# Optimization experiments

Measured on AMD Instinct MI355X. Metric: run time of the kernel, lower is better.

## Reference

```python
import jax, jax.numpy as jnp
import numpy as np

COMMITMENT = 1e-4
EPS = 1e-12  # F.normalize eps


def setup_inputs() -> dict:
    key = jax.random.key(0)
    k1, k2 = jax.random.split(key)
    b, h, l, d, c = 4, 8, 4096, 64, 512
    x = jax.random.normal(k1, (b, h, l, d), dtype=jnp.float32)
    means = jax.random.normal(k2, (h, c, d), dtype=jnp.float32)
    return {"x": x, "means": means}


def reference(x, means):
    # x: [b,h,l,d], means: [h,c,d]
    h = means.shape[0]
    # F.normalize(x, 2, dim=-1): x / max(||x||, eps)
    norm = jnp.linalg.norm(x, axis=-1, keepdims=True)
    xn = x / jnp.maximum(norm, EPS)
    # cosine similarity to cluster centers: [b,h,l,c]
    dists = jnp.einsum('bhld,hcd->bhlc', xn, means)
    buckets = jnp.argmax(dists, axis=-1)  # [b,h,l]
    # batched_index_select of means per (head, bucket): [b,h,l,d]
    routed_means = means[jnp.arange(h)[None, :, None], buckets]
    loss = jnp.mean((xn - routed_means) ** 2) * COMMITMENT
    return dists, loss
```

## Files before the change

### kernel.cpp

```cpp
#include <hip/hip_runtime.h>
#include <hip/hip_bf16.h>

#define NB 4
#define NH 8
#define NL 4096
#define ND 64
#define NC 512
#define TILE_L 64
#define EPSV 1e-12f
#define COMMITV 0.0001f
#define NBLOCKS (NB * NH * (NL / TILE_L))

typedef __attribute__((ext_vector_type(8))) short bf16x8;
typedef __attribute__((ext_vector_type(4))) float f32x4;

__device__ __forceinline__ unsigned bfpack(float a, float b) {
    unsigned ua = __float_as_uint(a);
    unsigned ub = __float_as_uint(b);
    ua = (ua + 0x7fffu + ((ua >> 16) & 1u)) >> 16;
    ub = (ub + 0x7fffu + ((ub >> 16) & 1u)) & 0xffff0000u;
    return (ua & 0xffffu) | ub;
}

__global__ __launch_bounds__(256, 2) void kmeans_kernel(
    const float* __restrict__ x, const float* __restrict__ means,
    float* __restrict__ dists, float* __restrict__ part)
{
    __shared__ alignas(16) unsigned short m_lds[NC * ND];
    __shared__ alignas(16) unsigned short x_lds[TILE_L * ND];
    __shared__ float msq[NC];
    __shared__ float sn2[TILE_L];
    __shared__ float wsum[4];

    const int t = threadIdx.x;
    const int ltiles = NL / TILE_L;
    const int bh = blockIdx.x / ltiles;
    const int l0 = (blockIdx.x % ltiles) * TILE_L;
    const int h  = bh & (NH - 1);

    const float4* mp = (const float4*)(means + (size_t)h * NC * ND);
    #pragma unroll 4
    for (int i = 0; i < 32; ++i) {
        int f4 = t + i * 256;
        float4 v = mp[f4];
        int row = f4 >> 4;
        int q = f4 & 15;
        float ss = v.x * v.x + v.y * v.y + v.z * v.z + v.w * v.w;
        ss += __shfl_xor(ss, 1); ss += __shfl_xor(ss, 2);
        ss += __shfl_xor(ss, 4); ss += __shfl_xor(ss, 8);
        if ((t & 15) == 0) msq[row] = ss;
        unsigned lo = bfpack(v.x, v.y), hi = bfpack(v.z, v.w);
        int byte = row * 128 + ((q * 8) ^ ((row & 7) << 4));
        *(unsigned long long*)((char*)m_lds + byte) =
            (unsigned long long)lo | ((unsigned long long)hi << 32);
    }

    const float4* xp = (const float4*)(x + ((size_t)bh * NL + l0) * ND);
    #pragma unroll
    for (int i = 0; i < 4; ++i) {
        int f4 = t + i * 256;
        float4 v = xp[f4];
        int row = f4 >> 4;
        int q = f4 & 15;
        float ss = v.x * v.x + v.y * v.y + v.z * v.z + v.w * v.w;
        ss += __shfl_xor(ss, 1); ss += __shfl_xor(ss, 2);
        ss += __shfl_xor(ss, 4); ss += __shfl_xor(ss, 8);
        float inv = 1.0f / fmaxf(sqrtf(ss), EPSV);
        if ((t & 15) == 0) sn2[row] = ss * inv * inv;
        float ax = v.x * inv, ay = v.y * inv, az = v.z * inv, aw = v.w * inv;
        int byte = row * 128 + ((q * 8) ^ ((row & 7) << 4));
        *(unsigned long long*)((char*)x_lds + byte) =
            (unsigned long long)bfpack(ax, ay) | ((unsigned long long)bfpack(az, aw) << 32);
    }
    __syncthreads();

    const int wave = t >> 6, lane = t & 63;
    const int r16 = lane & 15, g = lane >> 4;

    const int arow = wave * 16 + r16;
    const char* xb = (const char*)x_lds + arow * 128;
    const int sw = (arow & 7) << 4;
    bf16x8 a0 = *(const bf16x8*)(xb + ((g * 16) ^ sw));
    bf16x8 a1 = *(const bf16x8*)(xb + ((64 + g * 16) ^ sw));

    float mx[4]; int mi[4];
    #pragma unroll
    for (int r = 0; r < 4; ++r) { mx[r] = -1e30f; mi[r] = 0; }

    const size_t obase = ((size_t)bh * NL + l0 + wave * 16) * NC;

    #pragma unroll 4
    for (int c0 = 0; c0 < NC; c0 += 16) {
        int brow = c0 + r16;
        const char* mb = (const char*)m_lds + brow * 128;
        const int bsw = (brow & 7) << 4;
        bf16x8 b0 = *(const bf16x8*)(mb + ((g * 16) ^ bsw));
        bf16x8 b1 = *(const bf16x8*)(mb + ((64 + g * 16) ^ bsw));
        f32x4 acc = {0.f, 0.f, 0.f, 0.f};
        acc = __builtin_amdgcn_mfma_f32_16x16x32_bf16(a0, b0, acc, 0, 0, 0);
        acc = __builtin_amdgcn_mfma_f32_16x16x32_bf16(a1, b1, acc, 0, 0, 0);
        #pragma unroll
        for (int r = 0; r < 4; ++r) {
            float v = acc[r];
            dists[obase + (size_t)(g * 4 + r) * NC + (c0 + r16)] = v;
            if (v > mx[r]) { mx[r] = v; mi[r] = c0 + r16; }
        }
    }

    #pragma unroll
    for (int s = 1; s < 16; s <<= 1) {
        #pragma unroll
        for (int r = 0; r < 4; ++r) {
            float ov = __shfl_xor(mx[r], s);
            int   oi = __shfl_xor(mi[r], s);
            if (ov > mx[r] || (ov == mx[r] && oi < mi[r])) { mx[r] = ov; mi[r] = oi; }
        }
    }

    float sacc = 0.f;
    #pragma unroll
    for (int r = 0; r < 4; ++r)
        sacc += sn2[wave * 16 + g * 4 + r] - 2.f * mx[r] + msq[mi[r]];
    if (r16 != 0) sacc = 0.f;
    sacc += __shfl_xor(sacc, 16);
    sacc += __shfl_xor(sacc, 32);
    if (lane == 0) wsum[wave] = sacc;
    __syncthreads();
    if (t == 0) part[blockIdx.x] = wsum[0] + wsum[1] + wsum[2] + wsum[3];
}

__global__ __launch_bounds__(256) void loss_reduce(
    const float* __restrict__ part, float* __restrict__ loss)
{
    __shared__ float w[4];
    const int t = threadIdx.x;
    float s = 0.f;
    #pragma unroll
    for (int i = 0; i < NBLOCKS / 256; ++i) s += part[t + i * 256];
    s += __shfl_xor(s, 1);  s += __shfl_xor(s, 2);  s += __shfl_xor(s, 4);
    s += __shfl_xor(s, 8);  s += __shfl_xor(s, 16); s += __shfl_xor(s, 32);
    if ((t & 63) == 0) w[t >> 6] = s;
    __syncthreads();
    if (t == 0)
        loss[0] = (w[0] + w[1] + w[2] + w[3]) *
                  (COMMITV / (float)((size_t)NB * NH * NL * ND));
}

extern "C" void kernel_launch(void* const* d_in, const int* in_sizes, int n_in,
                              void* d_out, int out_size, void* d_ws, size_t ws_size,
                              hipStream_t stream) {
    const float* x = (const float*)d_in[0];
    const float* means = (const float*)d_in[1];
    float* dists = (float*)d_out;
    float* loss = dists + (size_t)NB * NH * NL * NC;
    float* part = (float*)d_ws;

    dim3 grid(NBLOCKS);
    dim3 block(256);
    kmeans_kernel<<<grid, block, 0, stream>>>(x, means, dists, part);
    loss_reduce<<<dim3(1), block, 0, stream>>>(part, loss);
}
```

Baseline: 362.3 us.

## Double L-tile per block, load x fragments directly to registers, nontemporal dists stores

Each block now covers 128 rows with 512 threads, which halves how often the per-head means tile is reloaded and converted into LDS. The x rows are read straight from global memory into MFMA A-fragments, normalised in registers with a cross-lane reduction, so the x LDS staging buffer is gone. The dists output is written with nontemporal stores to cut cache pollution from the large write stream. LDS use per block stays near 66KB, so occupancy may be limited, and the direct x loads are less coalesced.

Result: faster. 330.2 us (-8.9%).

```diff
diff --git a/kernel.cpp b/kernel.cpp
--- a/kernel.cpp
+++ b/kernel.cpp
@@ -6,10 +6,10 @@
 #define NL 4096
 #define ND 64
 #define NC 512
-#define TILE_L 64
+#define TILE_L 128
+#define NBLOCKS (NB * NH * (NL / TILE_L))
 #define EPSV 1e-12f
 #define COMMITV 0.0001f
-#define NBLOCKS (NB * NH * (NL / TILE_L))
 
 typedef __attribute__((ext_vector_type(8))) short bf16x8;
 typedef __attribute__((ext_vector_type(4))) float f32x4;
@@ -22,15 +22,15 @@
     return (ua & 0xffffu) | ub;
 }
 
-__global__ __launch_bounds__(256, 2) void kmeans_kernel(
+union bfrag { unsigned u[4]; bf16x8 v; };
+
+__global__ __launch_bounds__(512, 4) void kmeans_kernel(
     const float* __restrict__ x, const float* __restrict__ means,
     float* __restrict__ dists, float* __restrict__ part)
 {
     __shared__ alignas(16) unsigned short m_lds[NC * ND];
-    __shared__ alignas(16) unsigned short x_lds[TILE_L * ND];
     __shared__ float msq[NC];
-    __shared__ float sn2[TILE_L];
-    __shared__ float wsum[4];
+    __shared__ float wsum[8];
 
     const int t = threadIdx.x;
     const int ltiles = NL / TILE_L;
@@ -40,8 +40,8 @@
 
     const float4* mp = (const float4*)(means + (size_t)h * NC * ND);
     #pragma unroll 4
-    for (int i = 0; i < 32; ++i) {
-        int f4 = t + i * 256;
+    for (int i = 0; i < 16; ++i) {
+        int f4 = t + i * 512;
         float4 v = mp[f4];
         int row = f4 >> 4;
         int q = f4 & 15;
@@ -55,33 +55,31 @@
             (unsigned long long)lo | ((unsigned long long)hi << 32);
     }
 
-    const float4* xp = (const float4*)(x + ((size_t)bh * NL + l0) * ND);
-    #pragma unroll
-    for (int i = 0; i < 4; ++i) {
-        int f4 = t + i * 256;
-        float4 v = xp[f4];
-        int row = f4 >> 4;
-        int q = f4 & 15;
-        float ss = v.x * v.x + v.y * v.y + v.z * v.z + v.w * v.w;
-        ss += __shfl_xor(ss, 1); ss += __shfl_xor(ss, 2);
-        ss += __shfl_xor(ss, 4); ss += __shfl_xor(ss, 8);
-        float inv = 1.0f / fmaxf(sqrtf(ss), EPSV);
-        if ((t & 15) == 0) sn2[row] = ss * inv * inv;
-        float ax = v.x * inv, ay = v.y * inv, az = v.z * inv, aw = v.w * inv;
-        int byte = row * 128 + ((q * 8) ^ ((row & 7) << 4));
-        *(unsigned long long*)((char*)x_lds + byte) =
-            (unsigned long long)bfpack(ax, ay) | ((unsigned long long)bfpack(az, aw) << 32);
-    }
-    __syncthreads();
-
     const int wave = t >> 6, lane = t & 63;
     const int r16 = lane & 15, g = lane >> 4;
 
-    const int arow = wave * 16 + r16;
-    const char* xb = (const char*)x_lds + arow * 128;
-    const int sw = (arow & 7) << 4;
-    bf16x8 a0 = *(const bf16x8*)(xb + ((g * 16) ^ sw));
-    bf16x8 a1 = *(const bf16x8*)(xb + ((64 + g * 16) ^ sw));
+    const int xrow = l0 + wave * 16 + r16;
+    const float4* xr = (const float4*)(x + ((size_t)bh * NL + xrow) * ND);
+    float4 v0 = xr[g * 2], v1 = xr[g * 2 + 1];
+    float4 v2 = xr[8 + g * 2], v3 = xr[8 + g * 2 + 1];
+
+    float ss = v0.x*v0.x + v0.y*v0.y + v0.z*v0.z + v0.w*v0.w
+             + v1.x*v1.x + v1.y*v1.y + v1.z*v1.z + v1.w*v1.w
+             + v2.x*v2.x + v2.y*v2.y + v2.z*v2.z + v2.w*v2.w
+             + v3.x*v3.x + v3.y*v3.y + v3.z*v3.z + v3.w*v3.w;
+    ss += __shfl_xor(ss, 16);
+    ss += __shfl_xor(ss, 32);
+    const float inv = 1.0f / fmaxf(sqrtf(ss), EPSV);
+    const float sn2 = ss * inv * inv;
+
+    bfrag a0f, a1f;
+    a0f.u[0] = bfpack(v0.x * inv, v0.y * inv); a0f.u[1] = bfpack(v0.z * inv, v0.w * inv);
+    a0f.u[2] = bfpack(v1.x * inv, v1.y * inv); a0f.u[3] = bfpack(v1.z * inv, v1.w * inv);
+    a1f.u[0] = bfpack(v2.x * inv, v2.y * inv); a1f.u[1] = bfpack(v2.z * inv, v2.w * inv);
+    a1f.u[2] = bfpack(v3.x * inv, v3.y * inv); a1f.u[3] = bfpack(v3.z * inv, v3.w * inv);
+    const bf16x8 a0 = a0f.v, a1 = a1f.v;
+
+    __syncthreads();
 
     float mx[4]; int mi[4];
     #pragma unroll
@@ -102,7 +100,8 @@
         #pragma unroll
         for (int r = 0; r < 4; ++r) {
             float v = acc[r];
-            dists[obase + (size_t)(g * 4 + r) * NC + (c0 + r16)] = v;
+            __builtin_nontemporal_store(v,
+                &dists[obase + (size_t)(g * 4 + r) * NC + (c0 + r16)]);
             if (v > mx[r]) { mx[r] = v; mi[r] = c0 + r16; }
         }
     }
@@ -119,14 +118,21 @@
 
     float sacc = 0.f;
     #pragma unroll
-    for (int r = 0; r < 4; ++r)
-        sacc += sn2[wave * 16 + g * 4 + r] - 2.f * mx[r] + msq[mi[r]];
+    for (int r = 0; r < 4; ++r) {
+        float s2 = __shfl(sn2, g * 4 + r);
+        sacc += s2 - 2.f * mx[r] + msq[mi[r]];
+    }
     if (r16 != 0) sacc = 0.f;
     sacc += __shfl_xor(sacc, 16);
     sacc += __shfl_xor(sacc, 32);
     if (lane == 0) wsum[wave] = sacc;
     __syncthreads();
-    if (t == 0) part[blockIdx.x] = wsum[0] + wsum[1] + wsum[2] + wsum[3];
+    if (t == 0) {
+        float s = 0.f;
+        #pragma unroll
+        for (int w = 0; w < 8; ++w) s += wsum[w];
+        part[blockIdx.x] = s;
+    }
 }
 
 __global__ __launch_bounds__(256) void loss_reduce(
@@ -155,8 +161,6 @@
     float* loss = dists + (size_t)NB * NH * NL * NC;
     float* part = (float*)d_ws;
 
-    dim3 grid(NBLOCKS);
-    dim3 block(256);
-    kmeans_kernel<<<grid, block, 0, stream>>>(x, means, dists, part);
-    loss_reduce<<<dim3(1), block, 0, stream>>>(part, loss);
+    kmeans_kernel<<<dim3(NBLOCKS), dim3(512), 0, stream>>>(x, means, dists, part);
+    loss_reduce<<<dim3(1), dim3(256), 0, stream>>>(part, loss);
 }
```
